# Kernel tuning notes

Hardware: AMD Instinct MI355X
Metric: run time of the kernel (lower is better)

## Reference

```python
import jax, jax.numpy as jnp
import numpy as np

N = 256      # doc_length
V = 300      # embed_dim
H = 256      # GRU hidden size
VOCAB = 50000
FC = 512     # fc_hiddim
B = 64
SIGMA = 0.95


def setup_inputs() -> dict:
    key = jax.random.key(0)
    ks = jax.random.split(key, 14)
    g = lambda k, sh, sc: (jax.random.normal(k, sh, jnp.float32) * sc)
    return {
        "x": jax.random.randint(ks[0], (B, 2, N), 0, VOCAB),
        "embed": g(ks[1], (VOCAB, V), 0.1),
        "W_ih_f": g(ks[2], (3 * H, V), 0.05),
        "W_hh_f": g(ks[3], (3 * H, H), 0.05),
        "b_ih_f": jnp.zeros((3 * H,), jnp.float32),
        "b_hh_f": jnp.zeros((3 * H,), jnp.float32),
        "W_ih_b": g(ks[4], (3 * H, V), 0.05),
        "W_hh_b": g(ks[5], (3 * H, H), 0.05),
        "b_ih_b": jnp.zeros((3 * H,), jnp.float32),
        "b_hh_b": jnp.zeros((3 * H,), jnp.float32),
        "fc1_w": g(ks[6], (FC, 8 * H), 0.02),
        "fc1_b": jnp.zeros((FC,), jnp.float32),
        "fc2_w": g(ks[7], (1, FC), 0.05),
        "fc2_b": jnp.zeros((1,), jnp.float32),
    }


def _gru_dir(x_seq, W_ih, W_hh, b_ih, b_hh):
    # x_seq: [B, N, V] -> outputs [B, N, H] (torch nn.GRU gate math)
    xg = jnp.einsum('bnv,gv->bng', x_seq, W_ih) + b_ih  # [B,N,3H]
    xg = jnp.moveaxis(xg, 1, 0)                          # [N,B,3H]
    h0 = jnp.zeros((x_seq.shape[0], H), x_seq.dtype)

    def step(h, xgt):
        hg = h @ W_hh.T + b_hh
        xr, xz, xn = jnp.split(xgt, 3, axis=-1)
        hr, hz, hn = jnp.split(hg, 3, axis=-1)
        r = jax.nn.sigmoid(xr + hr)
        z = jax.nn.sigmoid(xz + hz)
        n = jnp.tanh(xn + r * hn)
        h_new = (1.0 - z) * n + z * h
        return h_new, h_new

    _, hs = jax.lax.scan(step, h0, xg)
    return jnp.moveaxis(hs, 0, 1)  # [B,N,H]


def _bigru(x_seq, W_ih_f, W_hh_f, b_ih_f, b_hh_f, W_ih_b, W_hh_b, b_ih_b, b_hh_b):
    fwd = _gru_dir(x_seq, W_ih_f, W_hh_f, b_ih_f, b_hh_f)
    bwd = _gru_dir(x_seq[:, ::-1], W_ih_b, W_hh_b, b_ih_b, b_hh_b)[:, ::-1]
    return jnp.concatenate([fwd, bwd], axis=-1)  # [B,N,2H]


def _attend_pool(o2, dist_bias):
    # o2: [B,N,D]; scores: [B,N,N] with squared-distance bias
    scores = jnp.einsum('bnd,bmd->bnm', o2, o2) - dist_bias
    a = jax.nn.softmax(scores, axis=2)
    o5 = jnp.einsum('bnm,bmd->bnd', a, o2)
    # avg/max pool over sequence -> [B, 2D]
    return jnp.concatenate([o5.mean(axis=1), o5.max(axis=1)], axis=1)


def reference(x, embed, W_ih_f, W_hh_f, b_ih_f, b_hh_f,
              W_ih_b, W_hh_b, b_ih_b, b_hh_b,
              fc1_w, fc1_b, fc2_w, fc2_b):
    emb = embed[x]  # [B,2,N,V]
    i = jnp.arange(N, dtype=jnp.float32)
    dist_bias = ((i[:, None] - i[None, :]) ** 2) / SIGMA  # [N,N]

    feats = []
    for s in range(2):  # the two documents of the pair
        o2 = _bigru(emb[:, s], W_ih_f, W_hh_f, b_ih_f, b_hh_f,
                    W_ih_b, W_hh_b, b_ih_b, b_hh_b)
        feats.append(_attend_pool(o2, dist_bias))
    o8a, o8b = feats

    z = jnp.concatenate([jnp.abs(o8a - o8b), o8a * o8b], axis=1)  # [B, 8H]
    h = jax.nn.relu(z @ fc1_w.T + fc1_b)
    out = jax.nn.sigmoid(h @ fc2_w.T + fc2_b)
    return out.reshape(-1)
```

## Files before the change

kernel.cpp:

```cpp
#include <hip/hip_runtime.h>
#include <hip/hip_bf16.h>

typedef __hip_bfloat16 bf16;
typedef __bf16 bf16x8 __attribute__((ext_vector_type(8)));
typedef float f32x4 __attribute__((ext_vector_type(4)));

#define SEQ 256
#define NB  64
#define NV  300
#define NH  256
#define G3  768
#define D2  512
#define LOG2E  1.44269504f
#define LOG2E2 2.88539008f

__device__ __forceinline__ ushort f2bs(float f){ __bf16 t = (__bf16)f; return *(ushort*)&t; }
__device__ __forceinline__ float u2f(uint u){ return __uint_as_float(u); }

__device__ __forceinline__ float ex2(float x){
#if __has_builtin(__builtin_amdgcn_exp2f)
  return __builtin_amdgcn_exp2f(x);
#else
  return __exp2f(x);
#endif
}
__device__ __forceinline__ float rcp_(float x){
#if __has_builtin(__builtin_amdgcn_rcpf)
  return __builtin_amdgcn_rcpf(x);
#else
  return 1.0f/x;
#endif
}

__device__ __forceinline__ void mm16(const float (*As)[68], const float (*Bs)[68],
                                     float acc[4][4], int ty, int tx){
  #pragma unroll
  for (int kk=0;kk<16;kk++){
    const float4 a4 = *(const float4*)&As[kk][ty*4];
    const float4 b4 = *(const float4*)&Bs[kk][tx*4];
    const float ai[4] = {a4.x,a4.y,a4.z,a4.w};
    const float bj[4] = {b4.x,b4.y,b4.z,b4.w};
    #pragma unroll
    for (int i=0;i<4;i++)
      #pragma unroll
      for (int j=0;j<4;j++)
        acc[i][j] = fmaf(ai[i], bj[j], acc[i][j]);
  }
}

__global__ __launch_bounds__(320) void k_emb(const int* __restrict__ x,
                                             const float* __restrict__ embed,
                                             ushort* __restrict__ E){
  const int t = threadIdx.x;
  const int rsub = t / 80, c4 = t - rsub*80;
  const int row = blockIdx.x*4 + rsub;
  const int s = row >> 14, b = (row >> 8) & 63, n = row & 255;
  const int token = x[(b*2 + s)*SEQ + n];
  const int k = c4*4;
  float4 v = make_float4(0,0,0,0);
  if (k < NV) v = *(const float4*)(embed + (size_t)token*NV + k);
  ushort4 o;
  o.x = f2bs(v.x); o.y = f2bs(v.y); o.z = f2bs(v.z); o.w = f2bs(v.w);
  *(ushort4*)(E + (size_t)row*320 + k) = o;
}

__global__ __launch_bounds__(320) void k_wih(const float* __restrict__ Wf,
                                             const float* __restrict__ Wb,
                                             ushort* __restrict__ W16){
  const int t = threadIdx.x;
  const int rsub = t / 80, c4 = t - rsub*80;
  const int g = blockIdx.x*4 + rsub;
  const int dir = g >= G3;
  const int gw = g - dir*G3;
  const float* __restrict__ W = dir ? Wb : Wf;
  const int k = c4*4;
  float4 v = make_float4(0,0,0,0);
  if (k < NV) v = *(const float4*)(W + (size_t)gw*NV + k);
  ushort4 o;
  o.x = f2bs(v.x); o.y = f2bs(v.y); o.z = f2bs(v.z); o.w = f2bs(v.w);
  *(ushort4*)(W16 + (size_t)g*320 + k) = o;
}

__global__ __launch_bounds__(256) void k_wpk(const float* __restrict__ Wf,
                                             const float* __restrict__ Wb,
                                             ushort* __restrict__ wpk){
  const int idx = blockIdx.x*256 + threadIdx.x;
  const int l   = idx & 63;
  const int kf  = (idx >> 6) & 7;
  const int r2  = idx >> 9;
  const int tau = r2 % 3;
  const int r3  = r2 / 3;
  const int w   = r3 & 15;
  const int dir = r3 >> 4;
  const int g   = tau*256 + w*16 + (l & 15);
  const int kb  = kf*32 + (l >> 4)*8;
  const float sc = (tau < 2) ? LOG2E : LOG2E2;
  const float* __restrict__ W = dir ? Wb : Wf;
  #pragma unroll
  for (int e=0;e<8;e++)
    wpk[(size_t)idx*8 + e] = f2bs(W[(size_t)g*NH + kb + e] * sc);
}

__global__ __launch_bounds__(256) void k_xgm(const ushort* __restrict__ E,
    const ushort* __restrict__ W16,
    const float* __restrict__ bihf, const float* __restrict__ bihb,
    const float* __restrict__ bhhf, const float* __restrict__ bhhb,
    char* __restrict__ xgq)
{
  __shared__ __align__(16) char As[10240];
  __shared__ __align__(16) char Bs[10240];
  const int tid = threadIdx.x, w = tid >> 6, l = tid & 63, l15 = l & 15, lg = l >> 4;
  const int r0 = blockIdx.x * 128;
  const int c0 = blockIdx.y * 128;
  const int dir = (c0 >= G3);
  const int cw0 = c0 - dir*G3;
  const float* __restrict__ bih = dir ? bihb : bihf;
  const float* __restrict__ bhh = dir ? bhhb : bhhf;

  const int srow = tid >> 1, sc_ = (tid & 1)*32;
  f32x4 acc[2][8] = {};

  for (int ks = 0; ks < 10; ks++){
    const uint4 a0 = *(const uint4*)((const char*)E + (size_t)(r0+srow)*640 + ks*64 + sc_);
    const uint4 a1 = *(const uint4*)((const char*)E + (size_t)(r0+srow)*640 + ks*64 + sc_ + 16);
    const uint4 b0 = *(const uint4*)((const char*)W16 + (size_t)(c0+srow)*640 + ks*64 + sc_);
    const uint4 b1 = *(const uint4*)((const char*)W16 + (size_t)(c0+srow)*640 + ks*64 + sc_ + 16);
    __syncthreads();
    *(uint4*)&As[srow*80 + sc_] = a0;
    *(uint4*)&As[srow*80 + sc_ + 16] = a1;
    *(uint4*)&Bs[srow*80 + sc_] = b0;
    *(uint4*)&Bs[srow*80 + sc_ + 16] = b1;
    __syncthreads();
    bf16x8 am[2], bn[8];
    #pragma unroll
    for (int mm=0;mm<2;mm++) am[mm] = *(const bf16x8*)&As[(w*32 + mm*16 + l15)*80 + lg*16];
    #pragma unroll
    for (int nt=0;nt<8;nt++)  bn[nt] = *(const bf16x8*)&Bs[(nt*16 + l15)*80 + lg*16];
    #pragma unroll
    for (int mm=0;mm<2;mm++)
      #pragma unroll
      for (int nt=0;nt<8;nt++)
        acc[mm][nt] = __builtin_amdgcn_mfma_f32_16x16x32_bf16(am[mm], bn[nt], acc[mm][nt], 0,0,0);
  }

  #pragma unroll
  for (int nt=0;nt<8;nt++){
    const int cwb = cw0 + nt*16;
    const int tau = cwb >> 8;
    const int ub  = (cwb & 255) + l15;
    const float sc2 = (tau < 2) ? LOG2E : LOG2E2;
    const float bias = bih[cwb + l15] + ((tau < 2) ? bhh[cwb + l15] : 0.0f);
    #pragma unroll
    for (int mm=0;mm<2;mm++)
      #pragma unroll
      for (int j=0;j<4;j++){
        const int row = r0 + w*32 + mm*16 + lg*4 + j;
        const int s_ = row >> 14, b_ = (row >> 8) & 63, n_ = row & 255;
        const int blk = (s_*2 + dir)*16 + (b_ >> 2);
        char* dst = xgq + ((size_t)blk*256 + n_)*6144 + ((b_&3)*3 + tau)*512 + ub*2;
        *(ushort*)dst = f2bs((acc[mm][nt][j] + bias) * sc2);
      }
  }
}

#define HSTR 544
__global__ __launch_bounds__(1024, 4) void k_gru(const char* __restrict__ xgq,
      const ushort* __restrict__ wpk,
      const float* __restrict__ bhhf, const float* __restrict__ bhhb,
      ushort* __restrict__ o2b)
{
  __shared__ __align__(16) char SMEM[2*16*HSTR];
  const int tid = threadIdx.x, w = tid >> 6, l = tid & 63, l15 = l & 15, lg = l >> 4;
  const int wgid = blockIdx.x;
  const int chain = wgid >> 4, sl = wgid & 15;
  const int s = chain >> 1, dir = chain & 1;
  const int sb64 = s*64 + sl*4;
  const float* __restrict__ bhh = dir ? bhhb : bhhf;
  const char* wbg = (const char*)wpk + (size_t)(dir*16 + w) * 24576;

  bf16x8 Wr[3][8];
  #pragma unroll
  for (int tau=0; tau<3; tau++)
    #pragma unroll
    for (int kf=0; kf<8; kf++)
      Wr[tau][kf] = *(const bf16x8*)(wbg + (size_t)((tau*8 + kf)*64 + l)*16);

  const float bn = bhh[512 + w*16 + l15] * LOG2E2;

  for (int k = tid; k < 4352; k += 1024) ((float*)SMEM)[k] = 0.0f;

  const int n0 = dir ? 255 : 0;
  const int qstep = dir ? -6144 : 6144;
  const int ostep = dir ? -1024 : 1024;
  const char* qb = xgq + ((size_t)wgid*256 + n0)*6144 + lg*1536 + (w*16 + l15)*2;
  char* op = (char*)o2b + ((size_t)(sb64 + lg)*256 + n0)*1024 + dir*512 + (w*16 + l15)*2;

  const int aoff = l15*HSTR + lg*16;
  const int hwoff = lg*4*HSTR + (w*16 + l15)*2;
  float hpv = 0.0f;

  __syncthreads();

  #pragma unroll 1
  for (int t=0; t<SEQ; t++){
    const int cur = t & 1;
    const int hcur = cur*8704, hnxt = (cur^1)*8704;

    const ushort q0 = *(const ushort*)(qb);
    const ushort q1 = *(const ushort*)(qb + 512);
    const ushort q2 = *(const ushort*)(qb + 1024);
    qb += qstep;

    f32x4 C[3] = {};
    #pragma unroll
    for (int kf=0; kf<8; kf++){
      const bf16x8 a = *(const bf16x8*)&SMEM[hcur + aoff + kf*64];
      C[0] = __builtin_amdgcn_mfma_f32_16x16x32_bf16(a, Wr[0][kf], C[0], 0, 0, 0);
      C[1] = __builtin_amdgcn_mfma_f32_16x16x32_bf16(a, Wr[1][kf], C[1], 0, 0, 0);
      C[2] = __builtin_amdgcn_mfma_f32_16x16x32_bf16(a, Wr[2][kf], C[2], 0, 0, 0);
    }

    const float xr = u2f((uint)q0 << 16);
    const float xz = u2f((uint)q1 << 16);
    const float xn = u2f((uint)q2 << 16);
    const float r  = rcp_(1.0f + ex2(-(xr + C[0][0])));
    const float z  = rcp_(1.0f + ex2(-(xz + C[1][0])));
    const float e2 = ex2(xn + r*(C[2][0] + bn));
    const float nn = (e2 - 1.0f) * rcp_(e2 + 1.0f);
    const float h  = nn + z*(hpv - nn);
    hpv = h;
    const ushort hs = f2bs(h);
    *(ushort*)&SMEM[hnxt + hwoff] = hs;
    *(ushort*)op = hs;
    op += ostep;
    __syncthreads();
  }
}

__global__ __launch_bounds__(256) void k_tr(const ushort* __restrict__ o2b,
                                            ushort* __restrict__ o2t){
  __shared__ __align__(16) char Ts[64*144];
  const int t = threadIdx.x;
  const int sb = blockIdx.z;
  const int n0 = blockIdx.x*64, d0 = blockIdx.y*64;
  const char* src = (const char*)o2b + (size_t)sb*262144;
  char* dst = (char*)o2t + (size_t)sb*262144;
  const int r = t >> 3, ch = t & 7;
  #pragma unroll
  for (int p=0;p<2;p++){
    const int row = r + p*32;
    const uint4 v = *(const uint4*)(src + (size_t)(n0+row)*1024 + d0*2 + ch*16);
    *(uint4*)&Ts[row*144 + ch*16] = v;
  }
  __syncthreads();
  #pragma unroll
  for (int p=0;p<2;p++){
    const int d = r + p*32;
    uint o[4];
    #pragma unroll
    for (int i=0;i<4;i++){
      const uint lo = *(const ushort*)&Ts[(ch*8 + 2*i)*144 + d*2];
      const uint hi = *(const ushort*)&Ts[(ch*8 + 2*i + 1)*144 + d*2];
      o[i] = lo | (hi << 16);
    }
    *(uint4*)(dst + (size_t)(d0+d)*512 + n0*2 + ch*16) = *(uint4*)o;
  }
}

__global__ __launch_bounds__(256) void k_scores(const ushort* __restrict__ o2b,
                                                float* __restrict__ sc){
  __shared__ __align__(16) char As[64*144];
  __shared__ __align__(16) char Bs[64*144];
  const int tid = threadIdx.x, w = tid >> 6, l = tid & 63, l15 = l & 15, lg = l >> 4;
  const int sb = blockIdx.z;
  const int n0 = blockIdx.x*64, m0 = blockIdx.y*64;
  const char* ob = (const char*)o2b + (size_t)sb*262144;
  const int srow = tid >> 2, scf = (tid & 3)*16;
  f32x4 acc[4] = {};
  for (int it=0; it<8; it++){
    const int k0 = it*64;
    const uint4 a0 = *(const uint4*)(ob + (size_t)(n0+srow)*1024 + k0*2 + scf);
    const uint4 a1 = *(const uint4*)(ob + (size_t)(n0+srow)*1024 + k0*2 + scf + 64);
    const uint4 b0 = *(const uint4*)(ob + (size_t)(m0+srow)*1024 + k0*2 + scf);
    const uint4 b1 = *(const uint4*)(ob + (size_t)(m0+srow)*1024 + k0*2 + scf + 64);
    __syncthreads();
    *(uint4*)&As[srow*144 + scf] = a0;
    *(uint4*)&As[srow*144 + scf + 64] = a1;
    *(uint4*)&Bs[srow*144 + scf] = b0;
    *(uint4*)&Bs[srow*144 + scf + 64] = b1;
    __syncthreads();
    #pragma unroll
    for (int ks=0; ks<2; ks++){
      const bf16x8 a = *(const bf16x8*)&As[(w*16 + l15)*144 + ks*64 + lg*16];
      #pragma unroll
      for (int nt=0; nt<4; nt++){
        const bf16x8 b = *(const bf16x8*)&Bs[(nt*16 + l15)*144 + ks*64 + lg*16];
        acc[nt] = __builtin_amdgcn_mfma_f32_16x16x32_bf16(a, b, acc[nt], 0, 0, 0);
      }
    }
  }
  #pragma unroll
  for (int nt=0; nt<4; nt++)
    #pragma unroll
    for (int j=0; j<4; j++){
      const int n = n0 + w*16 + lg*4 + j;
      const int m = m0 + nt*16 + l15;
      const float d = (float)(n - m);
      sc[((size_t)sb*SEQ + n)*SEQ + m] = acc[nt][j] - d*d*(1.0f/0.95f);
    }
}

__global__ __launch_bounds__(256) void k_softmax(const float* __restrict__ sc,
                                                 ushort* __restrict__ P){
  const int row = blockIdx.x*4 + (threadIdx.x >> 6);
  const int lane = threadIdx.x & 63;
  const float4 v = *(const float4*)(sc + (size_t)row*SEQ + lane*4);
  float m = fmaxf(fmaxf(v.x,v.y), fmaxf(v.z,v.w));
  #pragma unroll
  for (int off=32; off; off>>=1) m = fmaxf(m, __shfl_xor(m, off));
  float4 e;
  e.x = __expf(v.x-m); e.y = __expf(v.y-m); e.z = __expf(v.z-m); e.w = __expf(v.w-m);
  float ssum = e.x+e.y+e.z+e.w;
  #pragma unroll
  for (int off=32; off; off>>=1) ssum += __shfl_xor(ssum, off);
  const float inv = 1.0f/ssum;
  uint2 o;
  o.x = (uint)f2bs(e.x*inv) | ((uint)f2bs(e.y*inv) << 16);
  o.y = (uint)f2bs(e.z*inv) | ((uint)f2bs(e.w*inv) << 16);
  *(uint2*)((char*)P + (size_t)row*512 + lane*8) = o;
}

__global__ __launch_bounds__(256) void k_o5(const ushort* __restrict__ P,
                                            const ushort* __restrict__ o2t,
                                            ushort* __restrict__ o5b){
  __shared__ __align__(16) char As[64*144];
  __shared__ __align__(16) char Bs[64*144];
  const int tid = threadIdx.x, w = tid >> 6, l = tid & 63, l15 = l & 15, lg = l >> 4;
  const int sb = blockIdx.z;
  const int n0 = blockIdx.x*64, d0 = blockIdx.y*64;
  const char* pa = (const char*)P + (size_t)sb*131072;
  const char* pb = (const char*)o2t + (size_t)sb*262144;
  const int srow = tid >> 2, scf = (tid & 3)*16;
  f32x4 acc[4] = {};
  for (int it=0; it<4; it++){
    const int k0 = it*64;
    const uint4 a0 = *(const uint4*)(pa + (size_t)(n0+srow)*512 + k0*2 + scf);
    const uint4 a1 = *(const uint4*)(pa + (size_t)(n0+srow)*512 + k0*2 + scf + 64);
    const uint4 b0 = *(const uint4*)(pb + (size_t)(d0+srow)*512 + k0*2 + scf);
    const uint4 b1 = *(const uint4*)(pb + (size_t)(d0+srow)*512 + k0*2 + scf + 64);
    __syncthreads();
    *(uint4*)&As[srow*144 + scf] = a0;
    *(uint4*)&As[srow*144 + scf + 64] = a1;
    *(uint4*)&Bs[srow*144 + scf] = b0;
    *(uint4*)&Bs[srow*144 + scf + 64] = b1;
    __syncthreads();
    #pragma unroll
    for (int ks=0; ks<2; ks++){
      const bf16x8 a = *(const bf16x8*)&As[(w*16 + l15)*144 + ks*64 + lg*16];
      #pragma unroll
      for (int nt=0; nt<4; nt++){
        const bf16x8 b = *(const bf16x8*)&Bs[(nt*16 + l15)*144 + ks*64 + lg*16];
        acc[nt] = __builtin_amdgcn_mfma_f32_16x16x32_bf16(a, b, acc[nt], 0, 0, 0);
      }
    }
  }
  #pragma unroll
  for (int nt=0; nt<4; nt++)
    #pragma unroll
    for (int j=0; j<4; j++){
      const int n = n0 + w*16 + lg*4 + j;
      const int d = d0 + nt*16 + l15;
      *(ushort*)((char*)o5b + (size_t)sb*262144 + (size_t)n*1024 + d*2) = f2bs(acc[nt][j]);
    }
}

__global__ __launch_bounds__(256) void k_pool(const ushort* __restrict__ o5b,
                                              float* __restrict__ feats){
  const int idx = blockIdx.x*256 + threadIdx.x;
  const int sb = idx >> 9, d = idx & 511;
  const ushort* __restrict__ Pp = o5b + (size_t)sb*SEQ*D2 + d;
  float sum = 0.0f, mx = -1e30f;
  for (int n=0;n<SEQ;n++){
    const float v = u2f(((uint)Pp[(size_t)n*D2]) << 16);
    sum += v; mx = fmaxf(mx, v);
  }
  feats[(size_t)sb*1024 + d] = sum*(1.0f/256.0f);
  feats[(size_t)sb*1024 + 512 + d] = mx;
}

__global__ __launch_bounds__(256) void k_z(const float* __restrict__ feats,
                                           float* __restrict__ Z){
  const int idx = blockIdx.x*256 + threadIdx.x;
  const int b = idx >> 11, k = idx & 2047;
  const int j = (k < 1024) ? k : (k - 1024);
  const float fa = feats[(size_t)b*1024 + j];
  const float fb = feats[(size_t)(64 + b)*1024 + j];
  Z[idx] = (k < 1024) ? fabsf(fa - fb) : fa*fb;
}

__global__ __launch_bounds__(256) void k_fc1(const float* __restrict__ Z,
                                             const float* __restrict__ w,
                                             const float* __restrict__ bias,
                                             float* __restrict__ h1){
  __shared__ float As[16][68];
  __shared__ float Bs[16][68];
  const int tid = threadIdx.x;
  const int c0 = blockIdx.x*64;
  const int lr = tid >> 2, lk = (tid & 3)*4;
  const int ty = tid >> 4, tx = tid & 15;
  float acc[4][4] = {};
  for (int k0=0;k0<2048;k0+=16){
    const float4 a = *(const float4*)(Z + (size_t)lr*2048 + k0 + lk);
    const float4 b = *(const float4*)(w + (size_t)(c0+lr)*2048 + k0 + lk);
    __syncthreads();
    As[lk+0][lr]=a.x; As[lk+1][lr]=a.y; As[lk+2][lr]=a.z; As[lk+3][lr]=a.w;
    Bs[lk+0][lr]=b.x; Bs[lk+1][lr]=b.y; Bs[lk+2][lr]=b.z; Bs[lk+3][lr]=b.w;
    __syncthreads();
    mm16(As, Bs, acc, ty, tx);
  }
  #pragma unroll
  for (int i=0;i<4;i++)
    #pragma unroll
    for (int j=0;j<4;j++)
      h1[(size_t)(ty*4+i)*512 + c0+tx*4+j] = fmaxf(acc[i][j] + bias[c0+tx*4+j], 0.0f);
}

__global__ __launch_bounds__(256) void k_fc2(const float* __restrict__ h1,
                                             const float* __restrict__ w2,
                                             const float* __restrict__ b2,
                                             float* __restrict__ out){
  __shared__ float red[256];
  const int b = blockIdx.x, tid = threadIdx.x;
  float p = h1[(size_t)b*512 + tid]*w2[tid] + h1[(size_t)b*512 + 256 + tid]*w2[256 + tid];
  red[tid] = p; __syncthreads();
  for (int s2=128; s2; s2>>=1){ if (tid < s2) red[tid] += red[tid+s2]; __syncthreads(); }
  if (tid == 0) out[b] = 1.0f/(1.0f + __expf(-(red[0] + b2[0])));
}

extern "C" void kernel_launch(void* const* d_in, const int* in_sizes, int n_in,
                              void* d_out, int out_size, void* d_ws, size_t ws_size,
                              hipStream_t stream){
  const int*   x     = (const int*)d_in[0];
  const float* embed = (const float*)d_in[1];
  const float* Wihf  = (const float*)d_in[2];
  const float* Whhf  = (const float*)d_in[3];
  const float* bihf  = (const float*)d_in[4];
  const float* bhhf  = (const float*)d_in[5];
  const float* Wihb  = (const float*)d_in[6];
  const float* Whhb  = (const float*)d_in[7];
  const float* bihb  = (const float*)d_in[8];
  const float* bhhb  = (const float*)d_in[9];
  const float* fc1w  = (const float*)d_in[10];
  const float* fc1b  = (const float*)d_in[11];
  const float* fc2w  = (const float*)d_in[12];
  const float* fc2b  = (const float*)d_in[13];
  float* out = (float*)d_out;

  char* ws = (char*)d_ws;
  char*   xgq    = ws;
  ushort* o2t    = (ushort*)ws;
  float*  scores = (float*)(ws + 33554432);
  ushort* P      = (ushort*)(ws + 67108864);
  ushort* o5b    = (ushort*)(ws + 83886080);
  ushort* E      = (ushort*)(ws + 100663296);
  ushort* o2b    = (ushort*)(ws + 121634816);
  ushort* W16    = (ushort*)(ws + 155189248);
  ushort* Wpk    = (ushort*)(ws + 156172288);
  float*  feats  = (float*)(ws + 156958720);
  float*  Z      = (float*)(ws + 157483008);
  float*  h1     = (float*)(ws + 158007296);

  k_emb<<<8192, 320, 0, stream>>>(x, embed, E);
  k_wih<<<384, 320, 0, stream>>>(Wihf, Wihb, W16);
  k_wpk<<<192, 256, 0, stream>>>(Whhf, Whhb, Wpk);
  k_xgm<<<dim3(256, 12), 256, 0, stream>>>(E, W16, bihf, bihb, bhhf, bhhb, xgq);
  k_gru<<<64, 1024, 0, stream>>>(xgq, Wpk, bhhf, bhhb, o2b);
  k_tr<<<dim3(4, 8, 128), 256, 0, stream>>>(o2b, o2t);
  k_scores<<<dim3(4, 4, 128), 256, 0, stream>>>(o2b, scores);
  k_softmax<<<8192, 256, 0, stream>>>(scores, P);
  k_o5<<<dim3(4, 8, 128), 256, 0, stream>>>(P, o2t, o5b);
  k_pool<<<256, 256, 0, stream>>>(o5b, feats);
  k_z<<<512, 256, 0, stream>>>(feats, Z);
  k_fc1<<<8, 256, 0, stream>>>(Z, fc1w, fc1b, h1);
  k_fc2<<<64, 256, 0, stream>>>(h1, fc2w, fc2b, out);
}
```

Measured before the change: 563.2 us.

## Software-pipeline GRU step: prefetch next gate inputs, defer output store, reorder MFMAs

The recurrent GRU loop now loads the next timestep's precomputed input-gate values one iteration ahead and defers the global store of h to the following iteration, so global memory latency is taken off the serial critical path. It also loads all LDS A-fragments up front and reorders the MFMA chains per gate (r, then z, then n), starting each gate's exp2 as soon as its accumulator is ready so transcendental work overlaps the remaining MFMAs. In exchange it uses more registers and adds branches inside the loop.

```diff
diff --git a/kernel.cpp b/kernel.cpp
--- a/kernel.cpp
+++ b/kernel.cpp
@@ -198,6 +198,12 @@
   const int aoff = l15*HSTR + lg*16;
   const int hwoff = lg*4*HSTR + (w*16 + l15)*2;
   float hpv = 0.0f;
+  ushort hsp = 0;
+
+  ushort qa0 = *(const ushort*)(qb);
+  ushort qa1 = *(const ushort*)(qb + 512);
+  ushort qa2 = *(const ushort*)(qb + 1024);
+  qb += qstep;
 
   __syncthreads();
 
@@ -206,35 +212,52 @@
     const int cur = t & 1;
     const int hcur = cur*8704, hnxt = (cur^1)*8704;
 
-    const ushort q0 = *(const ushort*)(qb);
-    const ushort q1 = *(const ushort*)(qb + 512);
-    const ushort q2 = *(const ushort*)(qb + 1024);
-    qb += qstep;
-
-    f32x4 C[3] = {};
-    #pragma unroll
-    for (int kf=0; kf<8; kf++){
-      const bf16x8 a = *(const bf16x8*)&SMEM[hcur + aoff + kf*64];
-      C[0] = __builtin_amdgcn_mfma_f32_16x16x32_bf16(a, Wr[0][kf], C[0], 0, 0, 0);
-      C[1] = __builtin_amdgcn_mfma_f32_16x16x32_bf16(a, Wr[1][kf], C[1], 0, 0, 0);
-      C[2] = __builtin_amdgcn_mfma_f32_16x16x32_bf16(a, Wr[2][kf], C[2], 0, 0, 0);
-    }
-
-    const float xr = u2f((uint)q0 << 16);
-    const float xz = u2f((uint)q1 << 16);
-    const float xn = u2f((uint)q2 << 16);
-    const float r  = rcp_(1.0f + ex2(-(xr + C[0][0])));
-    const float z  = rcp_(1.0f + ex2(-(xz + C[1][0])));
-    const float e2 = ex2(xn + r*(C[2][0] + bn));
+    ushort nq0 = 0, nq1 = 0, nq2 = 0;
+    if (t < 255){
+      nq0 = *(const ushort*)(qb);
+      nq1 = *(const ushort*)(qb + 512);
+      nq2 = *(const ushort*)(qb + 1024);
+      qb += qstep;
+    }
+    if (t){
+      *(ushort*)op = hsp;
+      op += ostep;
+    }
+
+    bf16x8 av[8];
+    #pragma unroll
+    for (int kf=0; kf<8; kf++)
+      av[kf] = *(const bf16x8*)&SMEM[hcur + aoff + kf*64];
+
+    f32x4 C0 = {}, C1 = {}, C2 = {};
+    #pragma unroll
+    for (int kf=0; kf<8; kf++)
+      C0 = __builtin_amdgcn_mfma_f32_16x16x32_bf16(av[kf], Wr[0][kf], C0, 0, 0, 0);
+    const float xr = u2f((uint)qa0 << 16);
+    const float r_e = ex2(-(xr + C0[0]));
+    #pragma unroll
+    for (int kf=0; kf<8; kf++)
+      C1 = __builtin_amdgcn_mfma_f32_16x16x32_bf16(av[kf], Wr[1][kf], C1, 0, 0, 0);
+    const float xz = u2f((uint)qa1 << 16);
+    const float z_e = ex2(-(xz + C1[0]));
+    #pragma unroll
+    for (int kf=0; kf<8; kf++)
+      C2 = __builtin_amdgcn_mfma_f32_16x16x32_bf16(av[kf], Wr[2][kf], C2, 0, 0, 0);
+
+    const float r  = rcp_(1.0f + r_e);
+    const float z  = rcp_(1.0f + z_e);
+    const float xn = u2f((uint)qa2 << 16);
+    const float e2 = ex2(xn + r*(C2[0] + bn));
     const float nn = (e2 - 1.0f) * rcp_(e2 + 1.0f);
     const float h  = nn + z*(hpv - nn);
     hpv = h;
     const ushort hs = f2bs(h);
+    hsp = hs;
     *(ushort*)&SMEM[hnxt + hwoff] = hs;
-    *(ushort*)op = hs;
-    op += ostep;
-    __syncthreads();
-  }
+    qa0 = nq0; qa1 = nq1; qa2 = nq2;
+    __syncthreads();
+  }
+  *(ushort*)op = hsp;
 }
 
 __global__ __launch_bounds__(256) void k_tr(const ushort* __restrict__ o2b,
```

New measurement: 625.3 us. 1.11x slower.

## Halve GRU workgroup to 8 waves, each wave owning two 16-column hidden tiles

Applied to the files above, without the earlier changes.

The recurrent GRU kernel now runs with 512 threads (8 waves) per workgroup instead of 1024. Each wave computes 32 hidden units (two 16-wide MFMA column tiles per gate) and holds twice as many W_hh fragments in registers. The recurrent weight packing kernel is reordered to match the new per-wave tile layout. The goal is cheaper per-step barriers with fewer waves and more MFMA work per wave between syncs, at the cost of higher register pressure and less parallelism across waves.

```diff
diff --git a/kernel.cpp b/kernel.cpp
--- a/kernel.cpp
+++ b/kernel.cpp
@@ -88,11 +88,12 @@
   const int l   = idx & 63;
   const int kf  = (idx >> 6) & 7;
   const int r2  = idx >> 9;
-  const int tau = r2 % 3;
-  const int r3  = r2 / 3;
-  const int w   = r3 & 15;
-  const int dir = r3 >> 4;
-  const int g   = tau*256 + w*16 + (l & 15);
+  const int nt  = r2 % 6;
+  const int r3  = r2 / 6;
+  const int w   = r3 & 7;
+  const int dir = r3 >> 3;
+  const int tau = nt >> 1, usub = nt & 1;
+  const int g   = tau*256 + w*32 + usub*16 + (l & 15);
   const int kb  = kf*32 + (l >> 4)*8;
   const float sc = (tau < 2) ? LOG2E : LOG2E2;
   const float* __restrict__ W = dir ? Wb : Wf;
@@ -164,7 +165,7 @@
 }
 
 #define HSTR 544
-__global__ __launch_bounds__(1024, 4) void k_gru(const char* __restrict__ xgq,
+__global__ __launch_bounds__(512, 2) void k_gru(const char* __restrict__ xgq,
       const ushort* __restrict__ wpk,
       const float* __restrict__ bhhf, const float* __restrict__ bhhb,
       ushort* __restrict__ o2b)
@@ -176,28 +177,31 @@
   const int s = chain >> 1, dir = chain & 1;
   const int sb64 = s*64 + sl*4;
   const float* __restrict__ bhh = dir ? bhhb : bhhf;
-  const char* wbg = (const char*)wpk + (size_t)(dir*16 + w) * 24576;
-
-  bf16x8 Wr[3][8];
-  #pragma unroll
-  for (int tau=0; tau<3; tau++)
+  const char* wbg = (const char*)wpk + (size_t)(dir*8 + w) * 49152;
+
+  bf16x8 Wr[6][8];
+  #pragma unroll
+  for (int nt=0; nt<6; nt++)
     #pragma unroll
     for (int kf=0; kf<8; kf++)
-      Wr[tau][kf] = *(const bf16x8*)(wbg + (size_t)((tau*8 + kf)*64 + l)*16);
-
-  const float bn = bhh[512 + w*16 + l15] * LOG2E2;
-
-  for (int k = tid; k < 4352; k += 1024) ((float*)SMEM)[k] = 0.0f;
+      Wr[nt][kf] = *(const bf16x8*)(wbg + (size_t)((nt*8 + kf)*64 + l)*16);
+
+  float bn2[2];
+  #pragma unroll
+  for (int usub=0; usub<2; usub++)
+    bn2[usub] = bhh[512 + w*32 + usub*16 + l15] * LOG2E2;
+
+  for (int k = tid; k < 4352; k += 512) ((float*)SMEM)[k] = 0.0f;
 
   const int n0 = dir ? 255 : 0;
   const int qstep = dir ? -6144 : 6144;
   const int ostep = dir ? -1024 : 1024;
-  const char* qb = xgq + ((size_t)wgid*256 + n0)*6144 + lg*1536 + (w*16 + l15)*2;
-  char* op = (char*)o2b + ((size_t)(sb64 + lg)*256 + n0)*1024 + dir*512 + (w*16 + l15)*2;
+  const char* qb = xgq + ((size_t)wgid*256 + n0)*6144 + lg*1536 + (w*32 + l15)*2;
+  char* op = (char*)o2b + ((size_t)(sb64 + lg)*256 + n0)*1024 + dir*512 + (w*32 + l15)*2;
 
   const int aoff = l15*HSTR + lg*16;
-  const int hwoff = lg*4*HSTR + (w*16 + l15)*2;
-  float hpv = 0.0f;
+  const int hwoff = lg*4*HSTR + (w*32 + l15)*2;
+  float hpv[2] = {0.0f, 0.0f};
 
   __syncthreads();
 
@@ -206,32 +210,38 @@
     const int cur = t & 1;
     const int hcur = cur*8704, hnxt = (cur^1)*8704;
 
-    const ushort q0 = *(const ushort*)(qb);
-    const ushort q1 = *(const ushort*)(qb + 512);
-    const ushort q2 = *(const ushort*)(qb + 1024);
+    ushort q[3][2];
+    #pragma unroll
+    for (int tau=0; tau<3; tau++){
+      q[tau][0] = *(const ushort*)(qb + tau*512);
+      q[tau][1] = *(const ushort*)(qb + tau*512 + 32);
+    }
     qb += qstep;
 
-    f32x4 C[3] = {};
+    f32x4 C[6] = {};
     #pragma unroll
     for (int kf=0; kf<8; kf++){
       const bf16x8 a = *(const bf16x8*)&SMEM[hcur + aoff + kf*64];
-      C[0] = __builtin_amdgcn_mfma_f32_16x16x32_bf16(a, Wr[0][kf], C[0], 0, 0, 0);
-      C[1] = __builtin_amdgcn_mfma_f32_16x16x32_bf16(a, Wr[1][kf], C[1], 0, 0, 0);
-      C[2] = __builtin_amdgcn_mfma_f32_16x16x32_bf16(a, Wr[2][kf], C[2], 0, 0, 0);
-    }
-
-    const float xr = u2f((uint)q0 << 16);
-    const float xz = u2f((uint)q1 << 16);
-    const float xn = u2f((uint)q2 << 16);
-    const float r  = rcp_(1.0f + ex2(-(xr + C[0][0])));
-    const float z  = rcp_(1.0f + ex2(-(xz + C[1][0])));
-    const float e2 = ex2(xn + r*(C[2][0] + bn));
-    const float nn = (e2 - 1.0f) * rcp_(e2 + 1.0f);
-    const float h  = nn + z*(hpv - nn);
-    hpv = h;
-    const ushort hs = f2bs(h);
-    *(ushort*)&SMEM[hnxt + hwoff] = hs;
-    *(ushort*)op = hs;
+      #pragma unroll
+      for (int nt=0; nt<6; nt++)
+        C[nt] = __builtin_amdgcn_mfma_f32_16x16x32_bf16(a, Wr[nt][kf], C[nt], 0, 0, 0);
+    }
+
+    #pragma unroll
+    for (int usub=0; usub<2; usub++){
+      const float xr = u2f((uint)q[0][usub] << 16);
+      const float xz = u2f((uint)q[1][usub] << 16);
+      const float xn = u2f((uint)q[2][usub] << 16);
+      const float r  = rcp_(1.0f + ex2(-(xr + C[usub][0])));
+      const float z  = rcp_(1.0f + ex2(-(xz + C[2+usub][0])));
+      const float e2 = ex2(xn + r*(C[4+usub][0] + bn2[usub]));
+      const float nn = (e2 - 1.0f) * rcp_(e2 + 1.0f);
+      const float h  = nn + z*(hpv[usub] - nn);
+      hpv[usub] = h;
+      const ushort hs = f2bs(h);
+      *(ushort*)&SMEM[hnxt + hwoff + usub*32] = hs;
+      *(ushort*)(op + usub*32) = hs;
+    }
     op += ostep;
     __syncthreads();
   }
@@ -474,7 +484,7 @@
   k_wih<<<384, 320, 0, stream>>>(Wihf, Wihb, W16);
   k_wpk<<<192, 256, 0, stream>>>(Whhf, Whhb, Wpk);
   k_xgm<<<dim3(256, 12), 256, 0, stream>>>(E, W16, bihf, bihb, bhhf, bhhb, xgq);
-  k_gru<<<64, 1024, 0, stream>>>(xgq, Wpk, bhhf, bhhb, o2b);
+  k_gru<<<64, 512, 0, stream>>>(xgq, Wpk, bhhf, bhhb, o2b);
   k_tr<<<dim3(4, 8, 128), 256, 0, stream>>>(o2b, o2t);
   k_scores<<<dim3(4, 4, 128), 256, 0, stream>>>(o2b, scores);
   k_softmax<<<8192, 256, 0, stream>>>(scores, P);
```

After: 583.1 us. +3.5%, slower.

## Fuse attention score GEMM with row softmax, dropping fp32 scores buffer

Applied to the files above, without the earlier changes.

Merges the score matmul and softmax kernels into a single kernel where each block computes a full 64x256 row strip of scores in registers, applies the distance bias, does the row max/sum with 16-lane shuffles, and writes bf16 probabilities directly. This removes the 32 MB fp32 scores round trip through global memory and one kernel launch. In exchange the grid shrinks from 2048 to 512 blocks, each holding 64 accumulator registers, and the P stores become scattered 2-byte writes, which may cost occupancy and store efficiency.

```diff
diff --git a/kernel.cpp b/kernel.cpp
--- a/kernel.cpp
+++ b/kernel.cpp
@@ -267,67 +267,82 @@
   }
 }
 
-__global__ __launch_bounds__(256) void k_scores(const ushort* __restrict__ o2b,
-                                                float* __restrict__ sc){
+__global__ __launch_bounds__(256) void k_sp(const ushort* __restrict__ o2b,
+                                            ushort* __restrict__ P){
   __shared__ __align__(16) char As[64*144];
   __shared__ __align__(16) char Bs[64*144];
   const int tid = threadIdx.x, w = tid >> 6, l = tid & 63, l15 = l & 15, lg = l >> 4;
-  const int sb = blockIdx.z;
-  const int n0 = blockIdx.x*64, m0 = blockIdx.y*64;
+  const int sb = blockIdx.y;
+  const int n0 = blockIdx.x*64;
   const char* ob = (const char*)o2b + (size_t)sb*262144;
   const int srow = tid >> 2, scf = (tid & 3)*16;
-  f32x4 acc[4] = {};
-  for (int it=0; it<8; it++){
-    const int k0 = it*64;
-    const uint4 a0 = *(const uint4*)(ob + (size_t)(n0+srow)*1024 + k0*2 + scf);
-    const uint4 a1 = *(const uint4*)(ob + (size_t)(n0+srow)*1024 + k0*2 + scf + 64);
-    const uint4 b0 = *(const uint4*)(ob + (size_t)(m0+srow)*1024 + k0*2 + scf);
-    const uint4 b1 = *(const uint4*)(ob + (size_t)(m0+srow)*1024 + k0*2 + scf + 64);
-    __syncthreads();
-    *(uint4*)&As[srow*144 + scf] = a0;
-    *(uint4*)&As[srow*144 + scf + 64] = a1;
-    *(uint4*)&Bs[srow*144 + scf] = b0;
-    *(uint4*)&Bs[srow*144 + scf + 64] = b1;
-    __syncthreads();
-    #pragma unroll
-    for (int ks=0; ks<2; ks++){
-      const bf16x8 a = *(const bf16x8*)&As[(w*16 + l15)*144 + ks*64 + lg*16];
+  f32x4 acc[4][4] = {};
+
+  #pragma unroll 1
+  for (int mt=0; mt<4; mt++){
+    const int m0 = mt*64;
+    #pragma unroll 1
+    for (int it=0; it<8; it++){
+      const int k0 = it*64;
+      const uint4 a0 = *(const uint4*)(ob + (size_t)(n0+srow)*1024 + k0*2 + scf);
+      const uint4 a1 = *(const uint4*)(ob + (size_t)(n0+srow)*1024 + k0*2 + scf + 64);
+      const uint4 b0 = *(const uint4*)(ob + (size_t)(m0+srow)*1024 + k0*2 + scf);
+      const uint4 b1 = *(const uint4*)(ob + (size_t)(m0+srow)*1024 + k0*2 + scf + 64);
+      __syncthreads();
+      *(uint4*)&As[srow*144 + scf] = a0;
+      *(uint4*)&As[srow*144 + scf + 64] = a1;
+      *(uint4*)&Bs[srow*144 + scf] = b0;
+      *(uint4*)&Bs[srow*144 + scf + 64] = b1;
+      __syncthreads();
+      #pragma unroll
+      for (int ks=0; ks<2; ks++){
+        const bf16x8 a = *(const bf16x8*)&As[(w*16 + l15)*144 + ks*64 + lg*16];
+        #pragma unroll
+        for (int nt=0; nt<4; nt++){
+          const bf16x8 b = *(const bf16x8*)&Bs[(nt*16 + l15)*144 + ks*64 + lg*16];
+          acc[mt][nt] = __builtin_amdgcn_mfma_f32_16x16x32_bf16(a, b, acc[mt][nt], 0, 0, 0);
+        }
+      }
+    }
+  }
+
+  ushort* Prow = P + (size_t)sb*65536;
+  #pragma unroll
+  for (int j=0; j<4; j++){
+    const int n = n0 + w*16 + lg*4 + j;
+    float mx = -1e30f;
+    #pragma unroll
+    for (int mt=0; mt<4; mt++)
       #pragma unroll
       for (int nt=0; nt<4; nt++){
-        const bf16x8 b = *(const bf16x8*)&Bs[(nt*16 + l15)*144 + ks*64 + lg*16];
-        acc[nt] = __builtin_amdgcn_mfma_f32_16x16x32_bf16(a, b, acc[nt], 0, 0, 0);
-      }
-    }
-  }
-  #pragma unroll
-  for (int nt=0; nt<4; nt++)
-    #pragma unroll
-    for (int j=0; j<4; j++){
-      const int n = n0 + w*16 + lg*4 + j;
-      const int m = m0 + nt*16 + l15;
-      const float d = (float)(n - m);
-      sc[((size_t)sb*SEQ + n)*SEQ + m] = acc[nt][j] - d*d*(1.0f/0.95f);
-    }
-}
-
-__global__ __launch_bounds__(256) void k_softmax(const float* __restrict__ sc,
-                                                 ushort* __restrict__ P){
-  const int row = blockIdx.x*4 + (threadIdx.x >> 6);
-  const int lane = threadIdx.x & 63;
-  const float4 v = *(const float4*)(sc + (size_t)row*SEQ + lane*4);
-  float m = fmaxf(fmaxf(v.x,v.y), fmaxf(v.z,v.w));
-  #pragma unroll
-  for (int off=32; off; off>>=1) m = fmaxf(m, __shfl_xor(m, off));
-  float4 e;
-  e.x = __expf(v.x-m); e.y = __expf(v.y-m); e.z = __expf(v.z-m); e.w = __expf(v.w-m);
-  float ssum = e.x+e.y+e.z+e.w;
-  #pragma unroll
-  for (int off=32; off; off>>=1) ssum += __shfl_xor(ssum, off);
-  const float inv = 1.0f/ssum;
-  uint2 o;
-  o.x = (uint)f2bs(e.x*inv) | ((uint)f2bs(e.y*inv) << 16);
-  o.y = (uint)f2bs(e.z*inv) | ((uint)f2bs(e.w*inv) << 16);
-  *(uint2*)((char*)P + (size_t)row*512 + lane*8) = o;
+        const int m = mt*64 + nt*16 + l15;
+        const float d = (float)(n - m);
+        const float v = acc[mt][nt][j] - d*d*(1.0f/0.95f);
+        acc[mt][nt][j] = v;
+        mx = fmaxf(mx, v);
+      }
+    #pragma unroll
+    for (int off=1; off<16; off<<=1) mx = fmaxf(mx, __shfl_xor(mx, off));
+    float ssum = 0.0f;
+    #pragma unroll
+    for (int mt=0; mt<4; mt++)
+      #pragma unroll
+      for (int nt=0; nt<4; nt++){
+        const float e = __expf(acc[mt][nt][j] - mx);
+        acc[mt][nt][j] = e;
+        ssum += e;
+      }
+    #pragma unroll
+    for (int off=1; off<16; off<<=1) ssum += __shfl_xor(ssum, off);
+    const float inv = 1.0f/ssum;
+    #pragma unroll
+    for (int mt=0; mt<4; mt++)
+      #pragma unroll
+      for (int nt=0; nt<4; nt++){
+        const int m = mt*64 + nt*16 + l15;
+        Prow[(size_t)n*256 + m] = f2bs(acc[mt][nt][j]*inv);
+      }
+  }
 }
 
 __global__ __launch_bounds__(256) void k_o5(const ushort* __restrict__ P,
@@ -459,7 +474,6 @@
   char* ws = (char*)d_ws;
   char*   xgq    = ws;
   ushort* o2t    = (ushort*)ws;
-  float*  scores = (float*)(ws + 33554432);
   ushort* P      = (ushort*)(ws + 67108864);
   ushort* o5b    = (ushort*)(ws + 83886080);
   ushort* E      = (ushort*)(ws + 100663296);
@@ -476,8 +490,7 @@
   k_xgm<<<dim3(256, 12), 256, 0, stream>>>(E, W16, bihf, bihb, bhhf, bhhb, xgq);
   k_gru<<<64, 1024, 0, stream>>>(xgq, Wpk, bhhf, bhhb, o2b);
   k_tr<<<dim3(4, 8, 128), 256, 0, stream>>>(o2b, o2t);
-  k_scores<<<dim3(4, 4, 128), 256, 0, stream>>>(o2b, scores);
-  k_softmax<<<8192, 256, 0, stream>>>(scores, P);
+  k_sp<<<dim3(4, 128), 256, 0, stream>>>(o2b, P);
   k_o5<<<dim3(4, 8, 128), 256, 0, stream>>>(P, o2t, o5b);
   k_pool<<<256, 256, 0, stream>>>(o5b, feats);
   k_z<<<512, 256, 0, stream>>>(feats, Z);
```

After: 653.8 us. 1.16x slower.
